# Performance work log

Hardware: AMD Instinct MI355X
Metric: run time of the kernel (lower is better)

The kernel has to match this reference:

```python
import jax, jax.numpy as jnp
import numpy as np

VOCAB = 32000
EMBED = 32
HIDDEN = 16
SEQ = 128
BATCH = 32


def setup_inputs() -> dict:
    key = jax.random.key(0)
    ks = jax.random.split(key, 10)
    stdv = 1.0 / np.sqrt(HIDDEN)
    u = lambda k, shape: jax.random.uniform(k, shape, jnp.float32, -stdv, stdv)
    return {
        "input_batch": jax.random.randint(ks[0], (SEQ, BATCH), 0, VOCAB),
        "embedding": u(ks[1], (VOCAB, EMBED)),
        "W_ih": u(ks[2], (4 * HIDDEN, EMBED)),
        "W_hh": u(ks[3], (4 * HIDDEN, HIDDEN)),
        "b_ih": u(ks[4], (4 * HIDDEN,)),
        "b_hh": u(ks[5], (4 * HIDDEN,)),
        "W_out": u(ks[6], (VOCAB, HIDDEN)),
        "b_out": u(ks[7], (VOCAB,)),
        "h0": jax.random.normal(ks[8], (BATCH, HIDDEN), jnp.float32),
        "c0": jax.random.normal(ks[9], (BATCH, HIDDEN), jnp.float32),
    }


def reference(input_batch, embedding, W_ih, W_hh, b_ih, b_hh, W_out, b_out, h0, c0):
    # input_batch: [S, B] int; returns log-probs [S, B, V]
    def step(carry, idx):
        h, c = carry
        x = embedding[idx]  # [B, E] gather
        gates = x @ W_ih.T + b_ih + h @ W_hh.T + b_hh  # [B, 4H]
        i, f, g, o = jnp.split(gates, 4, axis=-1)
        c_new = jax.nn.sigmoid(f) * c + jax.nn.sigmoid(i) * jnp.tanh(g)
        h_new = jax.nn.sigmoid(o) * jnp.tanh(c_new)
        logits = h_new @ W_out.T + b_out  # [B, V]
        return (h_new, c_new), jax.nn.log_softmax(logits, axis=-1)

    _, predictions = jax.lax.scan(step, (h0, c0), input_batch)
    return predictions
```

## Files before the change

### kernel.cpp

```cpp
#include <hip/hip_runtime.h>
#include <hip/hip_bf16.h>

#define VOCAB  32000
#define EMBED  32
#define HIDDEN 16
#define SEQ    128
#define BATCH  32

typedef __attribute__((ext_vector_type(8))) short short8;
typedef __attribute__((ext_vector_type(4))) float float4v;

#define LOG2E 1.4426950408889634f
#define LN2   0.6931471805599453f

__device__ __forceinline__ float fexp2(float x) { return __builtin_amdgcn_exp2f(x); }
__device__ __forceinline__ float frcp(float x)  { return __builtin_amdgcn_rcpf(x); }
__device__ __forceinline__ float flog2(float x) { return __builtin_amdgcn_logf(x); }

__device__ __forceinline__ unsigned short f2bf(float x) {
    unsigned u = __float_as_uint(x);
    unsigned r = u + 0x7fffu + ((u >> 16) & 1u);
    return (unsigned short)(r >> 16);
}

__global__ __launch_bounds__(256) void k_convert(
    const float* __restrict__ W_out, const float* __restrict__ b_out,
    unsigned short* __restrict__ Wo16, unsigned short* __restrict__ bo16)
{
    int t4 = (blockIdx.x * 256 + threadIdx.x) * 4;
    const int NW = VOCAB * HIDDEN;
    if (t4 < NW) {
        float4 v = *(const float4*)(W_out + t4);
        Wo16[t4 + 0] = f2bf(v.x); Wo16[t4 + 1] = f2bf(v.y);
        Wo16[t4 + 2] = f2bf(v.z); Wo16[t4 + 3] = f2bf(v.w);
    } else if (t4 < NW + VOCAB) {
        int j = t4 - NW;
        float4 v = *(const float4*)(b_out + j);
        bo16[j + 0] = f2bf(v.x); bo16[j + 1] = f2bf(v.y);
        bo16[j + 2] = f2bf(v.z); bo16[j + 3] = f2bf(v.w);
    }
}

__global__ __launch_bounds__(256) void k_proj(
    const float* __restrict__ emb,
    const float* __restrict__ W_ih,
    const float* __restrict__ b_ih,
    const float* __restrict__ b_hh,
    float* __restrict__ proj)
{
    int j  = threadIdx.x & 63;
    int vl = threadIdx.x >> 6;
    int vbase = blockIdx.x * 32 + vl * 8;

    float w[32];
    {
        const float4* wp = (const float4*)(W_ih + j * 32);
#pragma unroll
        for (int i = 0; i < 8; ++i) *((float4*)w + i) = wp[i];
    }
    float bias = b_ih[j] + b_hh[j];

#pragma unroll
    for (int r = 0; r < 8; ++r) {
        int v = vbase + r;
        float x[32];
        const float4* xp = (const float4*)(emb + v * 32);
#pragma unroll
        for (int i = 0; i < 8; ++i) *((float4*)x + i) = xp[i];
        float a0 = bias, a1 = 0.f;
#pragma unroll
        for (int i = 0; i < 16; ++i) {
            a0 += x[2*i]   * w[2*i];
            a1 += x[2*i+1] * w[2*i+1];
        }
        proj[(size_t)v * 64 + j] = a0 + a1;
    }
}

__global__ __launch_bounds__(64) void k_lstm(
    const int* __restrict__ idx,
    const float* __restrict__ proj,
    const float* __restrict__ W_hh,
    const float* __restrict__ h0,
    const float* __restrict__ c0,
    unsigned short* __restrict__ h_ws)
{
    int b = blockIdx.x;
    int j = threadIdx.x;

    float w[16];
    {
        const float4* wp = (const float4*)(W_hh + j * 16);
#pragma unroll
        for (int i = 0; i < 4; ++i) *((float4*)w + i) = wp[i];
    }

    int l15 = j & 15;
    float h = h0[b * HIDDEN + l15];
    float c = c0[b * HIDDEN + l15];

    int i0 = idx[j * BATCH + b];
    int i1 = idx[(j + 64) * BATCH + b];

    float xg0 = proj[(size_t)__shfl(i0, 0) * 64 + j];
    float xg1 = proj[(size_t)__shfl(i0, 1) * 64 + j];

    for (int s = 0; s < SEQ; ++s) {
        float xg = xg0;
        xg0 = xg1;
        if (s + 2 < SEQ) {
            int sn = s + 2;
            int idn = __shfl((sn < 64) ? i0 : i1, sn & 63);
            xg1 = proj[(size_t)idn * 64 + j];
        }

        float a0 = xg, a1 = 0.f;
#pragma unroll
        for (int k = 0; k < 8; ++k) {
            a0 += w[2*k]   * __shfl(h, 2*k);
            a1 += w[2*k+1] * __shfl(h, 2*k+1);
        }
        float acc = a0 + a1;

        float e1 = fexp2(-acc * LOG2E);
        float sg = frcp(1.f + e1);
        float e2 = fexp2(-2.f * acc * LOG2E);
        float th = 2.f * frcp(1.f + e2) - 1.f;
        float act = ((j >> 4) == 2) ? th : sg;

        float i_ = __shfl(act, l15);
        float f_ = __shfl(act, l15 + 16);
        float g_ = __shfl(act, l15 + 32);
        float o_ = __shfl(act, l15 + 48);

        c = f_ * c + i_ * g_;
        float e3 = fexp2(-2.f * c * LOG2E);
        float hc = 2.f * frcp(1.f + e3) - 1.f;
        h = o_ * hc;

        if (j < 16)
            h_ws[(size_t)(s * BATCH + b) * HIDDEN + j] = f2bf(h);
    }
}

__global__ __launch_bounds__(512) void k_logits(
    const unsigned short* __restrict__ Wo16,
    const unsigned short* __restrict__ bo16,
    const unsigned short* __restrict__ h_ws,
    float* __restrict__ out)
{
    __shared__ float sums[8][16];

    int r0   = blockIdx.x * 16;
    int tid  = threadIdx.x;
    int wave = tid >> 6;
    int lane = tid & 63;
    int n = lane & 15;
    int q = lane >> 4;

    short8 bfrag = {0, 0, 0, 0, 0, 0, 0, 0};
    if (q < 2)
        bfrag = *(const short8*)(h_ws + (size_t)(r0 + n) * 16 + 8 * q);
    else if (q == 2)
        bfrag[0] = (short)0x3F80;

    const int NT = VOCAB / (16 * 8);

    float s0 = 0.f, s1 = 0.f, s2 = 0.f, s3 = 0.f;

    short8 a_cur = {0, 0, 0, 0, 0, 0, 0, 0};
    {
        int v0 = wave * 16;
        if (q < 2)       a_cur = *(const short8*)(Wo16 + (size_t)(v0 + n) * 16 + 8 * q);
        else if (q == 2) a_cur[0] = (short)bo16[v0 + n];
    }
    for (int t = 0; t < NT; ++t) {
        short8 a_nxt = {0, 0, 0, 0, 0, 0, 0, 0};
        if (t + 1 < NT) {
            int v0 = ((t + 1) * 8 + wave) * 16;
            if (q < 2)       a_nxt = *(const short8*)(Wo16 + (size_t)(v0 + n) * 16 + 8 * q);
            else if (q == 2) a_nxt[0] = (short)bo16[v0 + n];
        }
        float4v dz = {0.f, 0.f, 0.f, 0.f};
        float4v d = __builtin_amdgcn_mfma_f32_16x16x32_bf16(a_cur, bfrag, dz, 0, 0, 0);
        s0 += fexp2(d[0] * LOG2E);
        s1 += fexp2(d[1] * LOG2E);
        s2 += fexp2(d[2] * LOG2E);
        s3 += fexp2(d[3] * LOG2E);
        a_cur = a_nxt;
    }
    float ssum = (s0 + s1) + (s2 + s3);
    ssum += __shfl_xor(ssum, 16);
    ssum += __shfl_xor(ssum, 32);
    if (q == 0) sums[wave][n] = ssum;
    __syncthreads();

    float tot = 0.f;
#pragma unroll
    for (int wv = 0; wv < 8; ++wv) tot += sums[wv][n];
    float K = flog2(tot) * LN2;

    {
        int v0 = wave * 16;
        short8 a0 = {0, 0, 0, 0, 0, 0, 0, 0};
        if (q < 2)       a0 = *(const short8*)(Wo16 + (size_t)(v0 + n) * 16 + 8 * q);
        else if (q == 2) a0[0] = (short)bo16[v0 + n];
        a_cur = a0;
    }
    size_t row_base = (size_t)(r0 + n) * VOCAB;
    for (int t = 0; t < NT; ++t) {
        short8 a_nxt = {0, 0, 0, 0, 0, 0, 0, 0};
        if (t + 1 < NT) {
            int v0 = ((t + 1) * 8 + wave) * 16;
            if (q < 2)       a_nxt = *(const short8*)(Wo16 + (size_t)(v0 + n) * 16 + 8 * q);
            else if (q == 2) a_nxt[0] = (short)bo16[v0 + n];
        }
        int v0 = (t * 8 + wave) * 16;
        float4v dz = {0.f, 0.f, 0.f, 0.f};
        float4v d = __builtin_amdgcn_mfma_f32_16x16x32_bf16(a_cur, bfrag, dz, 0, 0, 0);
        float4v ov;
        ov[0] = d[0] - K;
        ov[1] = d[1] - K;
        ov[2] = d[2] - K;
        ov[3] = d[3] - K;
        *(float4v*)(out + row_base + v0 + 4 * q) = ov;
        a_cur = a_nxt;
    }
}

extern "C" void kernel_launch(void* const* d_in, const int* in_sizes, int n_in,
                              void* d_out, int out_size, void* d_ws, size_t ws_size,
                              hipStream_t stream)
{
    const int*   idx   = (const int*)d_in[0];
    const float* emb   = (const float*)d_in[1];
    const float* W_ih  = (const float*)d_in[2];
    const float* W_hh  = (const float*)d_in[3];
    const float* b_ih  = (const float*)d_in[4];
    const float* b_hh  = (const float*)d_in[5];
    const float* W_out = (const float*)d_in[6];
    const float* b_out = (const float*)d_in[7];
    const float* h0    = (const float*)d_in[8];
    const float* c0    = (const float*)d_in[9];

    char* p = (char*)d_ws;
    float*          proj = (float*)p;                      p += (size_t)VOCAB * 64 * 4;
    unsigned short* Wo16 = (unsigned short*)p;             p += (size_t)VOCAB * 16 * 2;
    unsigned short* bo16 = (unsigned short*)p;             p += (size_t)VOCAB * 2;
    unsigned short* h_ws = (unsigned short*)p;

    const int NCVT = (VOCAB * HIDDEN + VOCAB) / 4;
    k_convert<<<(NCVT + 255) / 256, 256, 0, stream>>>(W_out, b_out, Wo16, bo16);
    k_proj<<<VOCAB / 32, 256, 0, stream>>>(emb, W_ih, b_ih, b_hh, proj);
    k_lstm<<<BATCH, 64, 0, stream>>>(idx, proj, W_hh, h0, c0, h_ws);
    k_logits<<<(SEQ * BATCH) / 16, 512, 0, stream>>>(Wo16, bo16, h_ws, (float*)d_out);
}
```

Baseline: 779.4 us.

## Split logits over vocab slices with atomic logsumexp and separate write pass

Fuses the bf16 conversion and embedding projection kernels into one prep kernel that also zeroes a global sum buffer. The logits kernel is split into a sum-of-exponentials pass and a write pass, each spread over a 2D grid that adds vocab slices. Partial sums are combined with atomicAdd, so the grid grows from 256 blocks to 2560 and fills more of the GPU. The cost is an extra launch, recomputing the MFMA in both passes, and float atomics whose ordering is not deterministic.

```diff
diff --git a/kernel.cpp b/kernel.cpp
--- a/kernel.cpp
+++ b/kernel.cpp
@@ -13,6 +13,10 @@
 #define LOG2E 1.4426950408889634f
 #define LN2   0.6931471805599453f
 
+#define NSLICE 10
+#define TPB    200
+#define TPW    25
+
 __device__ __forceinline__ float fexp2(float x) { return __builtin_amdgcn_exp2f(x); }
 __device__ __forceinline__ float frcp(float x)  { return __builtin_amdgcn_rcpf(x); }
 __device__ __forceinline__ float flog2(float x) { return __builtin_amdgcn_logf(x); }
@@ -23,57 +27,63 @@
     return (unsigned short)(r >> 16);
 }
 
-__global__ __launch_bounds__(256) void k_convert(
-    const float* __restrict__ W_out, const float* __restrict__ b_out,
-    unsigned short* __restrict__ Wo16, unsigned short* __restrict__ bo16)
-{
-    int t4 = (blockIdx.x * 256 + threadIdx.x) * 4;
-    const int NW = VOCAB * HIDDEN;
-    if (t4 < NW) {
-        float4 v = *(const float4*)(W_out + t4);
-        Wo16[t4 + 0] = f2bf(v.x); Wo16[t4 + 1] = f2bf(v.y);
-        Wo16[t4 + 2] = f2bf(v.z); Wo16[t4 + 3] = f2bf(v.w);
-    } else if (t4 < NW + VOCAB) {
-        int j = t4 - NW;
-        float4 v = *(const float4*)(b_out + j);
-        bo16[j + 0] = f2bf(v.x); bo16[j + 1] = f2bf(v.y);
-        bo16[j + 2] = f2bf(v.z); bo16[j + 3] = f2bf(v.w);
-    }
-}
-
-__global__ __launch_bounds__(256) void k_proj(
+__global__ __launch_bounds__(256) void k_prep(
     const float* __restrict__ emb,
     const float* __restrict__ W_ih,
     const float* __restrict__ b_ih,
     const float* __restrict__ b_hh,
-    float* __restrict__ proj)
-{
-    int j  = threadIdx.x & 63;
-    int vl = threadIdx.x >> 6;
-    int vbase = blockIdx.x * 32 + vl * 8;
-
-    float w[32];
-    {
-        const float4* wp = (const float4*)(W_ih + j * 32);
-#pragma unroll
-        for (int i = 0; i < 8; ++i) *((float4*)w + i) = wp[i];
-    }
-    float bias = b_ih[j] + b_hh[j];
-
-#pragma unroll
-    for (int r = 0; r < 8; ++r) {
-        int v = vbase + r;
-        float x[32];
-        const float4* xp = (const float4*)(emb + v * 32);
-#pragma unroll
-        for (int i = 0; i < 8; ++i) *((float4*)x + i) = xp[i];
-        float a0 = bias, a1 = 0.f;
-#pragma unroll
-        for (int i = 0; i < 16; ++i) {
-            a0 += x[2*i]   * w[2*i];
-            a1 += x[2*i+1] * w[2*i+1];
-        }
-        proj[(size_t)v * 64 + j] = a0 + a1;
+    float* __restrict__ proj,
+    const float* __restrict__ W_out,
+    const float* __restrict__ b_out,
+    unsigned short* __restrict__ Wo16,
+    unsigned short* __restrict__ bo16,
+    float* __restrict__ gsum)
+{
+    int bx = blockIdx.x;
+    if (bx < 1000) {
+        int j  = threadIdx.x & 63;
+        int vl = threadIdx.x >> 6;
+        int vbase = bx * 32 + vl * 8;
+
+        float w[32];
+        {
+            const float4* wp = (const float4*)(W_ih + j * 32);
+#pragma unroll
+            for (int i = 0; i < 8; ++i) *((float4*)w + i) = wp[i];
+        }
+        float bias = b_ih[j] + b_hh[j];
+
+#pragma unroll
+        for (int r = 0; r < 8; ++r) {
+            int v = vbase + r;
+            float x[32];
+            const float4* xp = (const float4*)(emb + v * 32);
+#pragma unroll
+            for (int i = 0; i < 8; ++i) *((float4*)x + i) = xp[i];
+            float a0 = bias, a1 = 0.f;
+#pragma unroll
+            for (int i = 0; i < 16; ++i) {
+                a0 += x[2*i]   * w[2*i];
+                a1 += x[2*i+1] * w[2*i+1];
+            }
+            proj[(size_t)v * 64 + j] = a0 + a1;
+        }
+    } else if (bx < 1532) {
+        int t4 = ((bx - 1000) * 256 + threadIdx.x) * 4;
+        const int NW = VOCAB * HIDDEN;
+        if (t4 < NW) {
+            float4 v = *(const float4*)(W_out + t4);
+            Wo16[t4 + 0] = f2bf(v.x); Wo16[t4 + 1] = f2bf(v.y);
+            Wo16[t4 + 2] = f2bf(v.z); Wo16[t4 + 3] = f2bf(v.w);
+        } else if (t4 < NW + VOCAB) {
+            int j = t4 - NW;
+            float4 v = *(const float4*)(b_out + j);
+            bo16[j + 0] = f2bf(v.x); bo16[j + 1] = f2bf(v.y);
+            bo16[j + 2] = f2bf(v.z); bo16[j + 3] = f2bf(v.w);
+        }
+    } else {
+        int i = (bx - 1532) * 256 + threadIdx.x;
+        ((float4*)gsum)[i] = make_float4(0.f, 0.f, 0.f, 0.f);
     }
 }
 
@@ -143,11 +153,11 @@
     }
 }
 
-__global__ __launch_bounds__(512) void k_logits(
+__global__ __launch_bounds__(512) void k_lse(
     const unsigned short* __restrict__ Wo16,
     const unsigned short* __restrict__ bo16,
     const unsigned short* __restrict__ h_ws,
-    float* __restrict__ out)
+    float* __restrict__ gsum)
 {
     __shared__ float sums[8][16];
 
@@ -164,20 +174,19 @@
     else if (q == 2)
         bfrag[0] = (short)0x3F80;
 
-    const int NT = VOCAB / (16 * 8);
+    int t0 = blockIdx.y * TPB + wave * TPW;
 
     float s0 = 0.f, s1 = 0.f, s2 = 0.f, s3 = 0.f;
-
     short8 a_cur = {0, 0, 0, 0, 0, 0, 0, 0};
     {
-        int v0 = wave * 16;
+        int v0 = t0 * 16;
         if (q < 2)       a_cur = *(const short8*)(Wo16 + (size_t)(v0 + n) * 16 + 8 * q);
         else if (q == 2) a_cur[0] = (short)bo16[v0 + n];
     }
-    for (int t = 0; t < NT; ++t) {
+    for (int t = 0; t < TPW; ++t) {
         short8 a_nxt = {0, 0, 0, 0, 0, 0, 0, 0};
-        if (t + 1 < NT) {
-            int v0 = ((t + 1) * 8 + wave) * 16;
+        if (t + 1 < TPW) {
+            int v0 = (t0 + t + 1) * 16;
             if (q < 2)       a_nxt = *(const short8*)(Wo16 + (size_t)(v0 + n) * 16 + 8 * q);
             else if (q == 2) a_nxt[0] = (short)bo16[v0 + n];
         }
@@ -195,27 +204,53 @@
     if (q == 0) sums[wave][n] = ssum;
     __syncthreads();
 
-    float tot = 0.f;
-#pragma unroll
-    for (int wv = 0; wv < 8; ++wv) tot += sums[wv][n];
-    float K = flog2(tot) * LN2;
-
+    if (tid < 16) {
+        float tot = 0.f;
+#pragma unroll
+        for (int wv = 0; wv < 8; ++wv) tot += sums[wv][tid];
+        atomicAdd(&gsum[r0 + tid], tot);
+    }
+}
+
+__global__ __launch_bounds__(512) void k_write(
+    const unsigned short* __restrict__ Wo16,
+    const unsigned short* __restrict__ bo16,
+    const unsigned short* __restrict__ h_ws,
+    const float* __restrict__ gsum,
+    float* __restrict__ out)
+{
+    int r0   = blockIdx.x * 16;
+    int tid  = threadIdx.x;
+    int wave = tid >> 6;
+    int lane = tid & 63;
+    int n = lane & 15;
+    int q = lane >> 4;
+
+    short8 bfrag = {0, 0, 0, 0, 0, 0, 0, 0};
+    if (q < 2)
+        bfrag = *(const short8*)(h_ws + (size_t)(r0 + n) * 16 + 8 * q);
+    else if (q == 2)
+        bfrag[0] = (short)0x3F80;
+
+    float K = flog2(gsum[r0 + n]) * LN2;
+
+    int t0 = blockIdx.y * TPB + wave * TPW;
+
+    short8 a_cur = {0, 0, 0, 0, 0, 0, 0, 0};
     {
-        int v0 = wave * 16;
-        short8 a0 = {0, 0, 0, 0, 0, 0, 0, 0};
-        if (q < 2)       a0 = *(const short8*)(Wo16 + (size_t)(v0 + n) * 16 + 8 * q);
-        else if (q == 2) a0[0] = (short)bo16[v0 + n];
-        a_cur = a0;
+        int v0 = t0 * 16;
+        if (q < 2)       a_cur = *(const short8*)(Wo16 + (size_t)(v0 + n) * 16 + 8 * q);
+        else if (q == 2) a_cur[0] = (short)bo16[v0 + n];
     }
     size_t row_base = (size_t)(r0 + n) * VOCAB;
-    for (int t = 0; t < NT; ++t) {
+    for (int t = 0; t < TPW; ++t) {
         short8 a_nxt = {0, 0, 0, 0, 0, 0, 0, 0};
-        if (t + 1 < NT) {
-            int v0 = ((t + 1) * 8 + wave) * 16;
+        if (t + 1 < TPW) {
+            int v0 = (t0 + t + 1) * 16;
             if (q < 2)       a_nxt = *(const short8*)(Wo16 + (size_t)(v0 + n) * 16 + 8 * q);
             else if (q == 2) a_nxt[0] = (short)bo16[v0 + n];
         }
-        int v0 = (t * 8 + wave) * 16;
+        int v0 = (t0 + t) * 16;
         float4v dz = {0.f, 0.f, 0.f, 0.f};
         float4v d = __builtin_amdgcn_mfma_f32_16x16x32_bf16(a_cur, bfrag, dz, 0, 0, 0);
         float4v ov;
@@ -247,11 +282,13 @@
     float*          proj = (float*)p;                      p += (size_t)VOCAB * 64 * 4;
     unsigned short* Wo16 = (unsigned short*)p;             p += (size_t)VOCAB * 16 * 2;
     unsigned short* bo16 = (unsigned short*)p;             p += (size_t)VOCAB * 2;
-    unsigned short* h_ws = (unsigned short*)p;
-
-    const int NCVT = (VOCAB * HIDDEN + VOCAB) / 4;
-    k_convert<<<(NCVT + 255) / 256, 256, 0, stream>>>(W_out, b_out, Wo16, bo16);
-    k_proj<<<VOCAB / 32, 256, 0, stream>>>(emb, W_ih, b_ih, b_hh, proj);
+    unsigned short* h_ws = (unsigned short*)p;             p += (size_t)SEQ * BATCH * HIDDEN * 2;
+    float*          gsum = (float*)p;
+
+    k_prep<<<1536, 256, 0, stream>>>(emb, W_ih, b_ih, b_hh, proj,
+                                     W_out, b_out, Wo16, bo16, gsum);
     k_lstm<<<BATCH, 64, 0, stream>>>(idx, proj, W_hh, h0, c0, h_ws);
-    k_logits<<<(SEQ * BATCH) / 16, 512, 0, stream>>>(Wo16, bo16, h_ws, (float*)d_out);
-}
+    dim3 g(SEQ * BATCH / 16, NSLICE);
+    k_lse<<<g, 512, 0, stream>>>(Wo16, bo16, h_ws, gsum);
+    k_write<<<g, 512, 0, stream>>>(Wo16, bo16, h_ws, gsum, (float*)d_out);
+}
```

Result: faster. 729.0 us (-6.5%).
